# Performance work log

Hardware: AMD Instinct MI355X
Metric: run time of the kernel (lower is better)

## Reference

```python
import jax, jax.numpy as jnp
import numpy as np

EPS = 1e-6      # zero-token detection eps
LN_EPS = 1e-5   # torch LayerNorm default
H = 8           # num_heads


def setup_inputs() -> dict:
    key = jax.random.key(0)
    ks = jax.random.split(key, 6)
    B, T, D = 4, 2048, 512
    embs = jax.random.normal(ks[0], (B, T, D), jnp.float32)
    labels = jax.random.uniform(ks[1], (B, T), jnp.float32)
    s = 1.0 / np.sqrt(D)
    ln_g = jnp.ones((D,), jnp.float32)
    ln_b = jnp.zeros((D,), jnp.float32)
    in_proj_w = jax.random.uniform(ks[2], (3 * D, D), jnp.float32, -s, s)
    in_proj_b = jnp.zeros((3 * D,), jnp.float32)
    out_w = jax.random.uniform(ks[3], (D, D), jnp.float32, -s, s)
    out_b = jnp.zeros((D,), jnp.float32)
    alpha = jnp.float32(1.0)
    beta = jnp.float32(0.0)
    return {"embs": embs, "labels": labels, "ln_g": ln_g, "ln_b": ln_b,
            "in_proj_w": in_proj_w, "in_proj_b": in_proj_b,
            "out_w": out_w, "out_b": out_b, "alpha": alpha, "beta": beta}


def reference(embs, labels, ln_g, ln_b, in_proj_w, in_proj_b, out_w, out_b, alpha, beta):
    B, T, D = embs.shape
    h, dh = H, D // H
    # pre-LayerNorm
    mu = embs.mean(-1, keepdims=True)
    var = ((embs - mu) ** 2).mean(-1, keepdims=True)
    x = (embs - mu) / jnp.sqrt(var + LN_EPS) * ln_g + ln_b
    # key padding mask from all-zero tokens (computed on normalized x, as in source)
    kpm = jnp.abs(x).sum(-1) <= EPS                      # [B,T] bool
    w = jnp.where(kpm, jnp.float32(0.0), labels)         # zero labels on masked tokens
    # fused qkv projection (nn.MultiheadAttention in_proj)
    qkv = x @ in_proj_w.T + in_proj_b                    # [B,T,3D]
    q, k, v = jnp.split(qkv, 3, axis=-1)
    def sp(a):
        return a.reshape(B, T, h, dh).transpose(0, 2, 1, 3)  # [B,h,T,dh]
    q, k, v = sp(q), sp(k), sp(v)
    scores = jnp.einsum('bhqd,bhkd->bhqk', q, k) / np.sqrt(dh)
    # additive label bias: alpha * labels (broadcast over heads & queries) + beta
    scores = scores + (alpha * w[:, None, None, :] + beta)
    # key padding mask -> -inf (use large negative for stability)
    scores = jnp.where(kpm[:, None, None, :], jnp.float32(-1e30), scores)
    a = jax.nn.softmax(scores, axis=-1)
    o = jnp.einsum('bhqk,bhkd->bhqd', a, v).transpose(0, 2, 1, 3).reshape(B, T, D)
    o = o @ out_w.T + out_b
    o = jnp.nan_to_num(o, nan=0.0, posinf=0.0, neginf=0.0)
    # masked mean pool over T
    m = (~kpm)[..., None].astype(o.dtype)                # [B,T,1]
    pooled = (o * m).sum(1) / jnp.maximum(m.sum(1), 1.0)  # [B,D]
    return pooled
```

## Files before the change

kernel.cpp:

```cpp
#include <hip/hip_runtime.h>
#include <math.h>

#define T 2048
#define D 512
#define NH 8
#define DH 64
#define NB 4
#define NTOK (NB * T)
#define LOG2E 1.44269504f
#define QSCALE (0.125f * LOG2E)

using bf16x8 = __attribute__((ext_vector_type(8))) short;
using f32x4  = __attribute__((ext_vector_type(4))) float;

static __device__ __forceinline__ unsigned short f2bf(float f) {
    union { float f; unsigned u; } v; v.f = f;
    unsigned r = v.u + 0x7fffu + ((v.u >> 16) & 1u);
    return (unsigned short)(r >> 16);
}
#if __has_builtin(__builtin_amdgcn_cvt_pk_bf16_f32)
static __device__ __forceinline__ unsigned pack_bf16_pair(float a, float b) {
    auto r = __builtin_amdgcn_cvt_pk_bf16_f32(a, b);
    union { decltype(r) v; unsigned u; } c; c.v = r;
    return c.u;
}
#else
static __device__ __forceinline__ unsigned pack_bf16_pair(float a, float b) {
    union { float f; unsigned u; } ua, ub; ua.f = a; ub.f = b;
    unsigned ra = ua.u + 0x7fffu + ((ua.u >> 16) & 1u);
    unsigned rb = ub.u + 0x7fffu + ((ub.u >> 16) & 1u);
    return __builtin_amdgcn_perm(rb, ra, 0x07060302);
}
#endif


__global__ __launch_bounds__(256) void ln_kernel(
    const float* __restrict__ embs, const float* __restrict__ labels,
    const float* __restrict__ g, const float* __restrict__ bb,
    const float* __restrict__ alpha_p, const float* __restrict__ beta_p,
    unsigned short* __restrict__ xfrag, float* __restrict__ wexp,
    float* __restrict__ kpmf)
{
    __shared__ __align__(16) unsigned short Xs[16][520];
    int tid = threadIdx.x, wave = tid >> 6, lane = tid & 63;
    int quad = lane >> 4, lm = lane & 15;
    int t16 = blockIdx.x;

    float4 g0 = *(const float4*)(g + lane * 8), g1 = *(const float4*)(g + lane * 8 + 4);
    float4 c0 = *(const float4*)(bb + lane * 8), c1 = *(const float4*)(bb + lane * 8 + 4);
    float gv[8] = {g0.x, g0.y, g0.z, g0.w, g1.x, g1.y, g1.z, g1.w};
    float cv[8] = {c0.x, c0.y, c0.z, c0.w, c1.x, c1.y, c1.z, c1.w};

    for (int tt = 0; tt < 4; ++tt) {
        int n = t16 * 16 + wave * 4 + tt;
        const float* e = embs + (size_t)n * D + lane * 8;
        float4 a4 = *(const float4*)e, b4 = *(const float4*)(e + 4);
        float v[8] = {a4.x, a4.y, a4.z, a4.w, b4.x, b4.y, b4.z, b4.w};

        float s = 0.f, ss = 0.f;
        #pragma unroll
        for (int j = 0; j < 8; ++j) { s += v[j]; ss += v[j] * v[j]; }
        #pragma unroll
        for (int o = 1; o <= 32; o <<= 1) {
            s += __shfl_xor(s, o, 64);
            ss += __shfl_xor(ss, o, 64);
        }
        float mu = s * (1.0f / D);
        float var = ss * (1.0f / D) - mu * mu;
        float rstd = rsqrtf(var + 1e-5f);

        float x[8], as = 0.f;
        #pragma unroll
        for (int j = 0; j < 8; ++j) {
            x[j] = (v[j] - mu) * rstd * gv[j] + cv[j];
            as += fabsf(x[j]);
        }
        uint4 pk;
        pk.x = pack_bf16_pair(x[0], x[1]);
        pk.y = pack_bf16_pair(x[2], x[3]);
        pk.z = pack_bf16_pair(x[4], x[5]);
        pk.w = pack_bf16_pair(x[6], x[7]);
        *(uint4*)&Xs[wave * 4 + tt][lane * 8] = pk;

        #pragma unroll
        for (int o = 1; o <= 32; o <<= 1) as += __shfl_xor(as, o, 64);
        if (lane == 0) {
            int kpm = (as <= 1e-6f);
            kpmf[n] = kpm ? 1.0f : 0.0f;
            wexp[n] = kpm ? 0.0f : __expf(alpha_p[0] * labels[n] + beta_p[0]);
        }
    }
    __syncthreads();
    #pragma unroll
    for (int i = 0; i < 4; ++i) {
        int kc = wave * 4 + i;
        bf16x8 fr = *(const bf16x8*)&Xs[lm][kc * 32 + quad * 8];
        *(bf16x8*)(xfrag + ((size_t)(t16 * 16 + kc) * 64 + lane) * 8) = fr;
    }
}

__global__ __launch_bounds__(256) void wconv_kernel(
    const float* __restrict__ w, unsigned short* __restrict__ wbfrag)
{
    __shared__ __align__(16) unsigned short Ws[16][520];
    int tid = threadIdx.x, wave = tid >> 6, lane = tid & 63;
    int quad = lane >> 4, lm = lane & 15;
    int j16 = blockIdx.x;

    for (int tt = 0; tt < 4; ++tt) {
        int j = j16 * 16 + wave * 4 + tt;
        const float* wp = w + (size_t)j * D + lane * 8;
        float4 a4 = *(const float4*)wp, b4 = *(const float4*)(wp + 4);
        uint4 pk;
        pk.x = pack_bf16_pair(a4.x, a4.y);
        pk.y = pack_bf16_pair(a4.z, a4.w);
        pk.z = pack_bf16_pair(b4.x, b4.y);
        pk.w = pack_bf16_pair(b4.z, b4.w);
        *(uint4*)&Ws[wave * 4 + tt][lane * 8] = pk;
    }
    __syncthreads();
    #pragma unroll
    for (int i = 0; i < 4; ++i) {
        int kc = wave * 4 + i;
        bf16x8 fr = *(const bf16x8*)&Ws[lm][kc * 32 + quad * 8];
        *(bf16x8*)(wbfrag + ((size_t)(j16 * 16 + kc) * 64 + lane) * 8) = fr;
    }
}

__global__ __launch_bounds__(256) void wfrag_fill(
    const float* __restrict__ wexp, unsigned short* __restrict__ vfrag)
{
    int idx = blockIdx.x * 256 + threadIdx.x;
    int lane = idx & 63, chunk = idx >> 6;
    int kk = chunk & 1, t64 = (chunk >> 1) & 31, bh = chunk >> 6;
    int lm = lane & 15, quad = lane >> 4;
    int b_ = bh >> 3;
    size_t base = (((size_t)chunk * 5 + 4) * 64 + lane) * 8;
    if (lm == 0) {
        int key0 = t64 * 64 + kk * 32 + quad * 8;
        const float* wp = wexp + b_ * T + key0;
        unsigned short vv[8];
        #pragma unroll
        for (int e = 0; e < 8; ++e) vv[e] = f2bf(wp[e]);
        *(uint4*)(vfrag + base) = *(uint4*)vv;
    } else {
        uint4 z = {0u, 0u, 0u, 0u};
        *(uint4*)(vfrag + base) = z;
    }
}

__global__ __launch_bounds__(256) void qkv_mfma(
    const unsigned short* __restrict__ xfrag, const unsigned short* __restrict__ wbfrag,
    const float* __restrict__ bias, const float* __restrict__ wexp,
    unsigned short* __restrict__ qfrag, unsigned short* __restrict__ kfrag,
    unsigned short* __restrict__ vfrag)
{
    __shared__ __align__(16) unsigned short Ls[4][64][72];
    int tid = threadIdx.x;
    int wave = tid >> 6, lane = tid & 63, quad = lane >> 4, lm = lane & 15;
    int wr = wave >> 1, wc = wave & 1;
    int m0 = blockIdx.x * 128 + wr * 64;
    int j0 = blockIdx.y * 128 + wc * 64;
    int mt16 = m0 >> 4, jt16 = j0 >> 4;

    f32x4 acc[4][4];
    #pragma unroll
    for (int a = 0; a < 4; ++a)
        #pragma unroll
        for (int b = 0; b < 4; ++b) acc[a][b] = (f32x4){0.f,0.f,0.f,0.f};

    bf16x8 af0[4], bf0[4], af1[4], bf1[4];
    auto load_ab = [&](int kc, bf16x8 (&af)[4], bf16x8 (&bf)[4]) {
        #pragma unroll
        for (int mf = 0; mf < 4; ++mf)
            af[mf] = *(const bf16x8*)(xfrag + ((size_t)((mt16 + mf) * 16 + kc) * 64 + lane) * 8);
        #pragma unroll
        for (int nt = 0; nt < 4; ++nt)
            bf[nt] = *(const bf16x8*)(wbfrag + ((size_t)((jt16 + nt) * 16 + kc) * 64 + lane) * 8);
    };
    auto do_mfma = [&](bf16x8 (&af)[4], bf16x8 (&bf)[4]) {
        #pragma unroll
        for (int mf = 0; mf < 4; ++mf)
            #pragma unroll
            for (int nt = 0; nt < 4; ++nt)
                acc[mf][nt] = __builtin_amdgcn_mfma_f32_16x16x32_bf16(af[mf], bf[nt], acc[mf][nt], 0, 0, 0);
    };

    load_ab(0, af0, bf0);
    for (int kc = 0; kc < 16; kc += 2) {
        load_ab(kc + 1, af1, bf1);
        do_mfma(af0, bf0);
        load_ab((kc + 2) & 15, af0, bf0);
        do_mfma(af1, bf1);
    }

    int part = j0 >> 9;
    int h = (j0 & 511) >> 6;
    int b_ = m0 >> 11, tloc = m0 & (T - 1);
    int bh = b_ * NH + h;
    float bcol[4];
    #pragma unroll
    for (int nt = 0; nt < 4; ++nt) bcol[nt] = bias[j0 + nt * 16 + lm];

    if (part == 2) {
        float wv[4][4];
        #pragma unroll
        for (int mf = 0; mf < 4; ++mf)
            #pragma unroll
            for (int r = 0; r < 4; ++r)
                wv[mf][r] = wexp[b_ * T + tloc + mf * 16 + quad * 4 + r];
        #pragma unroll
        for (int mf = 0; mf < 4; ++mf)
            #pragma unroll
            for (int nt = 0; nt < 4; ++nt) {
                uint2 pw;
                pw.x = pack_bf16_pair((acc[mf][nt][0] + bcol[nt]) * wv[mf][0],
                                      (acc[mf][nt][1] + bcol[nt]) * wv[mf][1]);
                pw.y = pack_bf16_pair((acc[mf][nt][2] + bcol[nt]) * wv[mf][2],
                                      (acc[mf][nt][3] + bcol[nt]) * wv[mf][3]);
                *(uint2*)&Ls[wave][nt * 16 + lm][mf * 16 + quad * 4] = pw;
            }
        #pragma unroll
        for (int nt = 0; nt < 4; ++nt)
            #pragma unroll
            for (int kk = 0; kk < 2; ++kk) {
                bf16x8 fr = *(const bf16x8*)&Ls[wave][nt * 16 + lm][kk * 32 + quad * 8];
                size_t chunk = ((((size_t)bh * 32 + (tloc >> 6)) * 2 + kk) * 5) + nt;
                *(bf16x8*)(vfrag + chunk * 512 + lane * 8) = fr;
            }
    } else {
        float scale = (part == 0) ? QSCALE : 1.0f;
        #pragma unroll
        for (int mf = 0; mf < 4; ++mf)
            #pragma unroll
            for (int nt = 0; nt < 4; ++nt)
                #pragma unroll
                for (int r = 0; r < 4; ++r)
                    Ls[wave][mf * 16 + quad * 4 + r][nt * 16 + lm] =
                        f2bf((acc[mf][nt][r] + bcol[nt]) * scale);
        if (part == 0) {
            #pragma unroll
            for (int mf = 0; mf < 4; ++mf)
                #pragma unroll
                for (int kk = 0; kk < 2; ++kk) {
                    bf16x8 fr = *(const bf16x8*)&Ls[wave][mf * 16 + lm][kk * 32 + quad * 8];
                    size_t chunk = ((size_t)bh * 128 + (tloc >> 4) + mf) * 2 + kk;
                    *(bf16x8*)(qfrag + chunk * 512 + lane * 8) = fr;
                }
        } else {
            #pragma unroll
            for (int nta = 0; nta < 4; ++nta)
                #pragma unroll
                for (int kk = 0; kk < 2; ++kk) {
                    bf16x8 fr = *(const bf16x8*)&Ls[wave][lm * 4 + nta][kk * 32 + quad * 8];
                    size_t chunk = ((((size_t)bh * 32 + (tloc >> 6)) * 2 + kk) * 4) + nta;
                    *(bf16x8*)(kfrag + chunk * 512 + lane * 8) = fr;
                }
        }
    }
}

__global__ __launch_bounds__(256) void attn_mfma(
    const unsigned short* __restrict__ qfrag, const unsigned short* __restrict__ kfrag,
    const unsigned short* __restrict__ vfrag, const float* __restrict__ kpmf,
    float* __restrict__ S)
{
    __shared__ __align__(16) unsigned short Ps[128][72];
    int g = blockIdx.x;
    int bh = g & 31, q0 = (g >> 5) * 128;
    int tid = threadIdx.x, wave = tid >> 6, lane = tid & 63;
    int quad = lane >> 4, lm = lane & 15;
    int b_ = bh >> 3, h = bh & 7;

    bf16x8 qf[2][2];
    int t32 = (q0 >> 5) + wave;
    #pragma unroll
    for (int mf = 0; mf < 2; ++mf)
        #pragma unroll
        for (int kk = 0; kk < 2; ++kk)
            qf[mf][kk] = *(const bf16x8*)(qfrag +
                ((((size_t)(bh * 64 + t32) * 2 + mf) * 2 + kk) * 64 + lane) * 8);

    f32x4 accO[2][4], accL[2];
    #pragma unroll
    for (int mf = 0; mf < 2; ++mf) {
        #pragma unroll
        for (int nt = 0; nt < 4; ++nt) accO[mf][nt] = (f32x4){0.f,0.f,0.f,0.f};
        accL[mf] = (f32x4){0.f,0.f,0.f,0.f};
    }

    const unsigned short* kb = kfrag + (size_t)bh * 32 * 8 * 512 + (size_t)lane * 8;
    const unsigned short* vb = vfrag + (size_t)bh * 32 * 10 * 512 + (size_t)lane * 8;

    bf16x8 kf0[4][2], kf1[4][2];
    auto load_k = [&](int t64, bf16x8 (&kf)[4][2]) {
        const unsigned short* p = kb + (size_t)t64 * 8 * 512;
        #pragma unroll
        for (int kk = 0; kk < 2; ++kk)
            #pragma unroll
            for (int nt = 0; nt < 4; ++nt)
                kf[nt][kk] = *(const bf16x8*)(p + ((size_t)kk * 4 + nt) * 512);
    };

    auto process = [&](int t64, bf16x8 (&kf)[4][2]) {
        const unsigned short* p = vb + (size_t)t64 * 10 * 512;
        bf16x8 vf[5][2];
        #pragma unroll
        for (int kk = 0; kk < 2; ++kk)
            #pragma unroll
            for (int nt = 0; nt < 5; ++nt)
                vf[nt][kk] = *(const bf16x8*)(p + ((size_t)kk * 5 + nt) * 512);

        f32x4 s[2][4];
        #pragma unroll
        for (int mf = 0; mf < 2; ++mf)
            #pragma unroll
            for (int nt = 0; nt < 4; ++nt) {
                f32x4 t0 = (f32x4){0.f,0.f,0.f,0.f};
                t0 = __builtin_amdgcn_mfma_f32_16x16x32_bf16(qf[mf][0], kf[nt][0], t0, 0, 0, 0);
                t0 = __builtin_amdgcn_mfma_f32_16x16x32_bf16(qf[mf][1], kf[nt][1], t0, 0, 0, 0);
                s[mf][nt] = t0;
            }

        #pragma unroll
        for (int mf = 0; mf < 2; ++mf) {
            int rowb = wave * 32 + mf * 16 + quad * 4;
            #pragma unroll
            for (int r = 0; r < 4; ++r) {
                float p0 = __builtin_amdgcn_exp2f(s[mf][0][r]);
                float p1 = __builtin_amdgcn_exp2f(s[mf][1][r]);
                float p2 = __builtin_amdgcn_exp2f(s[mf][2][r]);
                float p3 = __builtin_amdgcn_exp2f(s[mf][3][r]);
                uint2 pw;
                pw.x = pack_bf16_pair(p0, p1);
                pw.y = pack_bf16_pair(p2, p3);
                *(uint2*)&Ps[rowb + r][lm * 4] = pw;
            }
        }

        bf16x8 pf[2][2];
        #pragma unroll
        for (int mf = 0; mf < 2; ++mf)
            #pragma unroll
            for (int kk = 0; kk < 2; ++kk)
                pf[mf][kk] = *(const bf16x8*)&Ps[wave * 32 + mf * 16 + lm][kk * 32 + quad * 8];

        #pragma unroll
        for (int mf = 0; mf < 2; ++mf) {
            #pragma unroll
            for (int nt = 0; nt < 4; ++nt) {
                accO[mf][nt] = __builtin_amdgcn_mfma_f32_16x16x32_bf16(pf[mf][0], vf[nt][0], accO[mf][nt], 0, 0, 0);
                accO[mf][nt] = __builtin_amdgcn_mfma_f32_16x16x32_bf16(pf[mf][1], vf[nt][1], accO[mf][nt], 0, 0, 0);
            }
            accL[mf] = __builtin_amdgcn_mfma_f32_16x16x32_bf16(pf[mf][0], vf[4][0], accL[mf], 0, 0, 0);
            accL[mf] = __builtin_amdgcn_mfma_f32_16x16x32_bf16(pf[mf][1], vf[4][1], accL[mf], 0, 0, 0);
        }
    };

    load_k(0, kf0);
    for (int t64 = 0; t64 < 32; t64 += 2) {
        load_k(t64 + 1, kf1);
        process(t64, kf0);
        load_k((t64 + 2) & 31, kf0);
        process(t64 + 1, kf1);
    }

    float pooled[4] = {0.f, 0.f, 0.f, 0.f};
    #pragma unroll
    for (int mf = 0; mf < 2; ++mf)
        #pragma unroll
        for (int r = 0; r < 4; ++r) {
            int row = q0 + wave * 32 + mf * 16 + quad * 4 + r;
            float l = __shfl(accL[mf][r], lane & 48, 64);
            float w = (1.0f - kpmf[b_ * T + row]) / l;
            #pragma unroll
            for (int nt = 0; nt < 4; ++nt) pooled[nt] += accO[mf][nt][r] * w;
        }
    #pragma unroll
    for (int nt = 0; nt < 4; ++nt) {
        pooled[nt] += __shfl_xor(pooled[nt], 16, 64);
        pooled[nt] += __shfl_xor(pooled[nt], 32, 64);
    }
    if (quad == 0) {
        #pragma unroll
        for (int nt = 0; nt < 4; ++nt)
            atomicAdd(&S[b_ * D + h * DH + nt * 16 + lm], pooled[nt]);
    }
}

__global__ __launch_bounds__(256) void out_kernel(
    const float* __restrict__ S, const float* __restrict__ kpmf,
    const float* __restrict__ Wo, const float* __restrict__ bo,
    float* __restrict__ out)
{
    __shared__ float Sl[512];
    __shared__ float cs[4];
    __shared__ float pr[4][64];
    int b_ = blockIdx.x >> 3;
    int cg = blockIdx.x & 7;
    int tid = threadIdx.x;
    int col = tid & 63, kq = tid >> 6;
    Sl[tid] = S[b_ * D + tid];
    Sl[tid + 256] = S[b_ * D + tid + 256];
    const float* kp = kpmf + b_ * T;
    float c = 0.f;
    for (int t = tid; t < T; t += 256) c += kp[t];
    #pragma unroll
    for (int o = 32; o; o >>= 1) c += __shfl_xor(c, o, 64);
    if ((tid & 63) == 0) cs[tid >> 6] = c;
    __syncthreads();
    float masked = cs[0] + cs[1] + cs[2] + cs[3];
    float cnt = (float)T - masked;
    float inv = 1.0f / fmaxf(cnt, 1.0f);

    int d = cg * 64 + col;
    const float4* wr4 = (const float4*)(Wo + (size_t)d * D + kq * 128);
    float dot = 0.f;
    #pragma unroll 8
    for (int i = 0; i < 32; ++i) {
        float4 w4 = wr4[i];
        int kbase = kq * 128 + i * 4;
        dot += Sl[kbase + 0] * w4.x + Sl[kbase + 1] * w4.y +
               Sl[kbase + 2] * w4.z + Sl[kbase + 3] * w4.w;
    }
    pr[kq][col] = dot;
    __syncthreads();
    if (kq == 0) {
        float tot = pr[0][col] + pr[1][col] + pr[2][col] + pr[3][col];
        out[b_ * D + d] = (tot + bo[d] * cnt) * inv;
    }
}

extern "C" void kernel_launch(void* const* d_in, const int* in_sizes, int n_in,
                              void* d_out, int out_size, void* d_ws, size_t ws_size,
                              hipStream_t stream) {
    const float* embs   = (const float*)d_in[0];
    const float* labels = (const float*)d_in[1];
    const float* ln_g   = (const float*)d_in[2];
    const float* ln_b   = (const float*)d_in[3];
    const float* ipw    = (const float*)d_in[4];
    const float* ipb    = (const float*)d_in[5];
    const float* ow     = (const float*)d_in[6];
    const float* obb    = (const float*)d_in[7];
    const float* alpha  = (const float*)d_in[8];
    const float* beta   = (const float*)d_in[9];
    float* out = (float*)d_out;

    unsigned short* xfrag  = (unsigned short*)d_ws;
    unsigned short* wbfrag = xfrag + (size_t)NTOK * D;
    unsigned short* qfrag  = wbfrag + (size_t)3 * D * D;
    unsigned short* kfrag  = qfrag + (size_t)NTOK * D;
    unsigned short* vfrag  = kfrag + (size_t)NTOK * D;
    float* wexp = (float*)(vfrag + (size_t)32 * 32 * 2 * 5 * 512);
    float* kpmf = wexp + NTOK;
    float* S    = kpmf + NTOK;

    hipMemsetAsync(S, 0, (size_t)NB * D * sizeof(float), stream);
    ln_kernel<<<NTOK / 16, 256, 0, stream>>>(embs, labels, ln_g, ln_b, alpha, beta,
                                             xfrag, wexp, kpmf);
    wconv_kernel<<<(3 * D) / 16, 256, 0, stream>>>(ipw, wbfrag);
    wfrag_fill<<<512, 256, 0, stream>>>(wexp, vfrag);
    dim3 gq(NTOK / 128, (3 * D) / 128);
    qkv_mfma<<<gq, 256, 0, stream>>>(xfrag, wbfrag, ipb, wexp, qfrag, kfrag, vfrag);
    attn_mfma<<<32 * (T / 128), 256, 0, stream>>>(qfrag, kfrag, vfrag, kpmf, S);
    out_kernel<<<NB * 8, 256, 0, stream>>>(S, kpmf, ow, obb, out);
}
```

Measured before the change: 173.2 us.

## Split attention keys across wave pairs with 64-row query tiles per wave

Each wave now handles 64 query rows instead of 32 and only half of the key sequence, with pairs of waves splitting the keys. The partial softmax denominators are combined through shared memory after a block barrier. This doubles reuse of each loaded K/V fragment per MFMA and halves the K/V traffic per wave. In exchange it raises register pressure (accO grows to 4x4) and adds an occupancy hint of 2 blocks per SM via launch_bounds. Partial outputs from both key halves are still summed through the existing atomicAdd pooling.

```diff
diff --git a/kernel.cpp b/kernel.cpp
--- a/kernel.cpp
+++ b/kernel.cpp
@@ -260,30 +260,33 @@
     }
 }
 
-__global__ __launch_bounds__(256) void attn_mfma(
+__global__ __launch_bounds__(256, 2) void attn_mfma(
     const unsigned short* __restrict__ qfrag, const unsigned short* __restrict__ kfrag,
     const unsigned short* __restrict__ vfrag, const float* __restrict__ kpmf,
     float* __restrict__ S)
 {
-    __shared__ __align__(16) unsigned short Ps[128][72];
+    __shared__ __align__(16) unsigned short Ps[4][64][72];
+    __shared__ float Lx[2][2][64];
     int g = blockIdx.x;
     int bh = g & 31, q0 = (g >> 5) * 128;
     int tid = threadIdx.x, wave = tid >> 6, lane = tid & 63;
     int quad = lane >> 4, lm = lane & 15;
+    int qh = wave >> 1, ks = wave & 1;
+    int qbase = q0 + qh * 64;
     int b_ = bh >> 3, h = bh & 7;
 
-    bf16x8 qf[2][2];
-    int t32 = (q0 >> 5) + wave;
-    #pragma unroll
-    for (int mf = 0; mf < 2; ++mf)
+    bf16x8 qf[4][2];
+    int t16b = (qbase >> 4);
+    #pragma unroll
+    for (int mf = 0; mf < 4; ++mf)
         #pragma unroll
         for (int kk = 0; kk < 2; ++kk)
             qf[mf][kk] = *(const bf16x8*)(qfrag +
-                ((((size_t)(bh * 64 + t32) * 2 + mf) * 2 + kk) * 64 + lane) * 8);
-
-    f32x4 accO[2][4], accL[2];
-    #pragma unroll
-    for (int mf = 0; mf < 2; ++mf) {
+                (((size_t)(bh * 128 + t16b + mf) * 2 + kk) * 64 + lane) * 8);
+
+    f32x4 accO[4][4], accL[4];
+    #pragma unroll
+    for (int mf = 0; mf < 4; ++mf) {
         #pragma unroll
         for (int nt = 0; nt < 4; ++nt) accO[mf][nt] = (f32x4){0.f,0.f,0.f,0.f};
         accL[mf] = (f32x4){0.f,0.f,0.f,0.f};
@@ -291,6 +294,7 @@
 
     const unsigned short* kb = kfrag + (size_t)bh * 32 * 8 * 512 + (size_t)lane * 8;
     const unsigned short* vb = vfrag + (size_t)bh * 32 * 10 * 512 + (size_t)lane * 8;
+    int t0k = ks * 16;
 
     bf16x8 kf0[4][2], kf1[4][2];
     auto load_k = [&](int t64, bf16x8 (&kf)[4][2]) {
@@ -311,42 +315,39 @@
             for (int nt = 0; nt < 5; ++nt)
                 vf[nt][kk] = *(const bf16x8*)(p + ((size_t)kk * 5 + nt) * 512);
 
-        f32x4 s[2][4];
-        #pragma unroll
-        for (int mf = 0; mf < 2; ++mf)
+        #pragma unroll
+        for (int mf = 0; mf < 4; ++mf) {
+            f32x4 s[4];
             #pragma unroll
             for (int nt = 0; nt < 4; ++nt) {
                 f32x4 t0 = (f32x4){0.f,0.f,0.f,0.f};
                 t0 = __builtin_amdgcn_mfma_f32_16x16x32_bf16(qf[mf][0], kf[nt][0], t0, 0, 0, 0);
                 t0 = __builtin_amdgcn_mfma_f32_16x16x32_bf16(qf[mf][1], kf[nt][1], t0, 0, 0, 0);
-                s[mf][nt] = t0;
+                s[nt] = t0;
             }
-
-        #pragma unroll
-        for (int mf = 0; mf < 2; ++mf) {
-            int rowb = wave * 32 + mf * 16 + quad * 4;
+            int rowb = mf * 16 + quad * 4;
             #pragma unroll
             for (int r = 0; r < 4; ++r) {
-                float p0 = __builtin_amdgcn_exp2f(s[mf][0][r]);
-                float p1 = __builtin_amdgcn_exp2f(s[mf][1][r]);
-                float p2 = __builtin_amdgcn_exp2f(s[mf][2][r]);
-                float p3 = __builtin_amdgcn_exp2f(s[mf][3][r]);
+                float p0 = __builtin_amdgcn_exp2f(s[0][r]);
+                float p1 = __builtin_amdgcn_exp2f(s[1][r]);
+                float p2 = __builtin_amdgcn_exp2f(s[2][r]);
+                float p3 = __builtin_amdgcn_exp2f(s[3][r]);
                 uint2 pw;
                 pw.x = pack_bf16_pair(p0, p1);
                 pw.y = pack_bf16_pair(p2, p3);
-                *(uint2*)&Ps[rowb + r][lm * 4] = pw;
+                *(uint2*)&Ps[wave][rowb + r][lm * 4] = pw;
             }
         }
 
-        bf16x8 pf[2][2];
-        #pragma unroll
-        for (int mf = 0; mf < 2; ++mf)
+        bf16x8 pf[4][2];
+        #pragma unroll
+        for (int mf = 0; mf < 4; ++mf)
             #pragma unroll
             for (int kk = 0; kk < 2; ++kk)
-                pf[mf][kk] = *(const bf16x8*)&Ps[wave * 32 + mf * 16 + lm][kk * 32 + quad * 8];
-
-        #pragma unroll
-        for (int mf = 0; mf < 2; ++mf) {
+                pf[mf][kk] = *(const bf16x8*)&Ps[wave][mf * 16 + lm][kk * 32 + quad * 8];
+
+        #pragma unroll
+        for (int mf = 0; mf < 4; ++mf) {
             #pragma unroll
             for (int nt = 0; nt < 4; ++nt) {
                 accO[mf][nt] = __builtin_amdgcn_mfma_f32_16x16x32_bf16(pf[mf][0], vf[nt][0], accO[mf][nt], 0, 0, 0);
@@ -357,22 +358,31 @@
         }
     };
 
-    load_k(0, kf0);
-    for (int t64 = 0; t64 < 32; t64 += 2) {
-        load_k(t64 + 1, kf1);
-        process(t64, kf0);
-        load_k((t64 + 2) & 31, kf0);
-        process(t64 + 1, kf1);
-    }
+    load_k(t0k, kf0);
+    for (int i = 0; i < 16; i += 2) {
+        load_k(t0k + i + 1, kf1);
+        process(t0k + i, kf0);
+        load_k(t0k + ((i + 2) & 15), kf0);
+        process(t0k + i + 1, kf1);
+    }
+
+    if (lm == 0) {
+        #pragma unroll
+        for (int mf = 0; mf < 4; ++mf)
+            #pragma unroll
+            for (int r = 0; r < 4; ++r)
+                Lx[qh][ks][mf * 16 + quad * 4 + r] = accL[mf][r];
+    }
+    __syncthreads();
 
     float pooled[4] = {0.f, 0.f, 0.f, 0.f};
     #pragma unroll
-    for (int mf = 0; mf < 2; ++mf)
+    for (int mf = 0; mf < 4; ++mf)
         #pragma unroll
         for (int r = 0; r < 4; ++r) {
-            int row = q0 + wave * 32 + mf * 16 + quad * 4 + r;
-            float l = __shfl(accL[mf][r], lane & 48, 64);
-            float w = (1.0f - kpmf[b_ * T + row]) / l;
+            int rloc = mf * 16 + quad * 4 + r;
+            float l = Lx[qh][0][rloc] + Lx[qh][1][rloc];
+            float w = (1.0f - kpmf[b_ * T + qbase + rloc]) / l;
             #pragma unroll
             for (int nt = 0; nt < 4; ++nt) pooled[nt] += accO[mf][nt][r] * w;
         }
```

New measurement: 165.7 us. 4.4% less time.
